# Kernel tuning notes

Measured on AMD Instinct MI355X. Metric: run time of the kernel, lower is better.

Reference implementation:

```python
import jax, jax.numpy as jnp
from jax import lax
import numpy as np

B, T, H, K = 128, 256, 768, 64


def setup_inputs() -> dict:
    key = jax.random.key(0)
    k1, k2, k3, k4 = jax.random.split(key, 4)
    hidden = jax.random.normal(k1, (B, T, H), dtype=jnp.float32)
    masks = jnp.ones((B, T), dtype=jnp.int32)
    target = jax.random.randint(k2, (B, T), 0, K, dtype=jnp.int32)
    W = jax.random.normal(k3, (H, K), dtype=jnp.float32) * 0.02
    b = jnp.zeros((K,), dtype=jnp.float32)
    transitions = jax.random.uniform(k4, (K, K), dtype=jnp.float32)
    return {"hidden": hidden, "masks": masks, "target": target,
            "W": W, "b": b, "transitions": transitions}


def _crf_log_norm(emissions, trans, seq_len):
    # emissions: [B,T,K]; forward algorithm (log-sum-exp recurrence over time)
    Tn = emissions.shape[1]
    alpha0 = emissions[:, 0]  # [B,K]

    def step(alpha, xs):
        emis_t, t = xs
        new = jax.nn.logsumexp(alpha[:, :, None] + trans[None], axis=1) + emis_t
        alpha = jnp.where((t < seq_len)[:, None], new, alpha)
        return alpha, None

    xs = (jnp.swapaxes(emissions[:, 1:], 0, 1), jnp.arange(1, Tn))
    alpha, _ = lax.scan(step, alpha0, xs)
    return jax.nn.logsumexp(alpha, axis=1)  # [B]


def _crf_sequence_score(emissions, tags, trans, seq_len):
    Tn = emissions.shape[1]
    t_idx = jnp.arange(Tn)
    valid = t_idx[None, :] < seq_len[:, None]  # [B,T]
    unary = jnp.take_along_axis(emissions, tags[..., None], axis=2)[..., 0]
    unary = jnp.sum(jnp.where(valid, unary, 0.0), axis=1)
    pair = trans[tags[:, :-1], tags[:, 1:]]  # [B,T-1]
    valid_pair = t_idx[1:][None, :] < seq_len[:, None]
    binary = jnp.sum(jnp.where(valid_pair, pair, 0.0), axis=1)
    return unary + binary


def _crf_decode(emissions, trans, seq_len):
    # Viterbi with backpointers; padded steps carry state (identity backptr)
    Bn, Tn, Kn = emissions.shape
    v0 = emissions[:, 0]

    def step(v, xs):
        emis_t, t = xs
        scores = v[:, :, None] + trans[None]  # [B, K_prev, K_cur]
        bp = jnp.argmax(scores, axis=1).astype(jnp.int32)
        new_v = jnp.max(scores, axis=1) + emis_t
        m = (t < seq_len)[:, None]
        v = jnp.where(m, new_v, v)
        bp = jnp.where(m, bp, jnp.arange(Kn, dtype=jnp.int32)[None])
        return v, bp

    xs = (jnp.swapaxes(emissions[:, 1:], 0, 1), jnp.arange(1, Tn))
    v, bps = lax.scan(step, v0, xs)  # bps: [T-1, B, K]
    best_score = jnp.max(v, axis=1)
    last_tag = jnp.argmax(v, axis=1).astype(jnp.int32)

    def back(tag, bp_t):
        prev = jnp.take_along_axis(bp_t, tag[:, None], axis=1)[:, 0]
        return prev, prev

    _, rev_tags = lax.scan(back, last_tag, bps, reverse=True)  # [T-1, B]
    path = jnp.concatenate([rev_tags, last_tag[None]], axis=0)  # [T, B]
    path = jnp.swapaxes(path, 0, 1)  # [B, T]
    valid = jnp.arange(Tn)[None, :] < seq_len[:, None]
    path = jnp.where(valid, path, 0)
    return path, best_score


def reference(hidden, masks, target, W, b, transitions):
    # dense projection (dropout omitted for determinism)
    emissions = jnp.einsum('bth,hk->btk', hidden, W) + b  # [B,T,K]
    seq_len = jnp.sum(masks, axis=1).astype(jnp.int32)
    log_norm = _crf_log_norm(emissions, transitions, seq_len)
    seq_score = _crf_sequence_score(emissions, target, transitions, seq_len)
    log_likelihood = seq_score - log_norm  # [B]
    decode_predict, _crf_scores = _crf_decode(emissions, transitions, seq_len)
    return decode_predict, log_likelihood
```

## Files before the change

### kernel.cpp

```cpp
#include <hip/hip_runtime.h>

#define B_ 128
#define T_ 256
#define H_ 768
#define K_ 64
#define BT_ (B_ * T_)

template <int CTRL>
__device__ __forceinline__ float dpp_mov_f(float x) {
    return __int_as_float(__builtin_amdgcn_update_dpp(
        __float_as_int(x), __float_as_int(x), CTRL, 0xF, 0xF, false));
}
__device__ __forceinline__ float wave_max64(float x) {
    x = fmaxf(x, dpp_mov_f<0x111>(x));
    x = fmaxf(x, dpp_mov_f<0x112>(x));
    x = fmaxf(x, dpp_mov_f<0x114>(x));
    x = fmaxf(x, dpp_mov_f<0x118>(x));
    x = fmaxf(x, dpp_mov_f<0x142>(x));
    x = fmaxf(x, dpp_mov_f<0x143>(x));
    return __int_as_float(__builtin_amdgcn_readlane(__float_as_int(x), 63));
}
__device__ __forceinline__ float readlane0_f(float x) {
    return __int_as_float(__builtin_amdgcn_readfirstlane(__float_as_int(x)));
}
template <int I>
__device__ __forceinline__ float readlane_f(float x) {
    return __int_as_float(__builtin_amdgcn_readlane(__float_as_int(x), I));
}

#define BK_ 32
#define BM_ 64
#define P_ 66
__global__ __launch_bounds__(256) void gemm_emis(const float* __restrict__ hidden,
                                                 const float* __restrict__ W,
                                                 const float* __restrict__ bias,
                                                 float* __restrict__ emis) {
    __shared__ float At[BK_ * P_];

    const int tid = threadIdx.x;
    const int lane = tid & 63;
    const int wc = __builtin_amdgcn_readfirstlane((tid >> 6) * 16);
    const int rowbase = blockIdx.x * BM_;
    const int srow = tid >> 2;
    const int scol = (tid & 3) * 8;

    float acc[16];
#pragma unroll
    for (int c = 0; c < 16; ++c) acc[c] = bias[wc + c];

    float4 pf0 = *(const float4*)&hidden[(size_t)(rowbase + srow) * H_ + scol];
    float4 pf1 = *(const float4*)&hidden[(size_t)(rowbase + srow) * H_ + scol + 4];

    for (int kb = 0; kb < H_ / BK_; ++kb) {
        __syncthreads();
        At[(scol + 0) * P_ + srow] = pf0.x;
        At[(scol + 1) * P_ + srow] = pf0.y;
        At[(scol + 2) * P_ + srow] = pf0.z;
        At[(scol + 3) * P_ + srow] = pf0.w;
        At[(scol + 4) * P_ + srow] = pf1.x;
        At[(scol + 5) * P_ + srow] = pf1.y;
        At[(scol + 6) * P_ + srow] = pf1.z;
        At[(scol + 7) * P_ + srow] = pf1.w;
        __syncthreads();
        if (kb + 1 < H_ / BK_) {
            pf0 = *(const float4*)&hidden[(size_t)(rowbase + srow) * H_ +
                                          (kb + 1) * BK_ + scol];
            pf1 = *(const float4*)&hidden[(size_t)(rowbase + srow) * H_ +
                                          (kb + 1) * BK_ + scol + 4];
        }
        const float* Wk = &W[(kb * BK_) * K_ + wc];
#pragma unroll 8
        for (int h = 0; h < BK_; ++h) {
            float a = At[h * P_ + lane];
            float4 w0 = *(const float4*)&Wk[h * K_ + 0];
            float4 w1 = *(const float4*)&Wk[h * K_ + 4];
            float4 w2 = *(const float4*)&Wk[h * K_ + 8];
            float4 w3 = *(const float4*)&Wk[h * K_ + 12];
            acc[0]  += a * w0.x;  acc[1]  += a * w0.y;
            acc[2]  += a * w0.z;  acc[3]  += a * w0.w;
            acc[4]  += a * w1.x;  acc[5]  += a * w1.y;
            acc[6]  += a * w1.z;  acc[7]  += a * w1.w;
            acc[8]  += a * w2.x;  acc[9]  += a * w2.y;
            acc[10] += a * w2.z;  acc[11] += a * w2.w;
            acc[12] += a * w3.x;  acc[13] += a * w3.y;
            acc[14] += a * w3.z;  acc[15] += a * w3.w;
        }
    }

    float* e = &emis[(size_t)(rowbase + lane) * K_ + wc];
#pragma unroll
    for (int q = 0; q < 4; ++q)
        *(float4*)&e[q * 4] = make_float4(acc[q * 4], acc[q * 4 + 1],
                                          acc[q * 4 + 2], acc[q * 4 + 3]);
}

__global__ __launch_bounds__(128, 1) void crf_kernel(const float* __restrict__ emis,
                                                     const int* __restrict__ masks,
                                                     const int* __restrict__ target,
                                                     const float* __restrict__ trans,
                                                     float* __restrict__ out) {
    __shared__ __align__(16) float ebuf[T_ * K_];
    __shared__ __align__(16) float vbuf[T_ * K_];
    __shared__ float tbuf[K_ * 65];

    const int tid = threadIdx.x;
    const int lane = tid & 63;
    const int b = blockIdx.x;
    const float* eb = emis + (size_t)b * (T_ * K_);

    {
        const float4* src = (const float4*)eb;
        float4* dst = (float4*)ebuf;
#pragma unroll
        for (int k = 0; k < 32; ++k) dst[tid + k * 128] = src[tid + k * 128];
    }
    int sl = 0;
#pragma unroll
    for (int k = 0; k < 4; ++k) sl += masks[b * T_ + lane + k * 64];
#pragma unroll
    for (int m = 32; m; m >>= 1) sl += __shfl_xor(sl, m, 64);
    const int seq_len = sl;
    __syncthreads();

    if (tid < 64) {
        float Ecol[64];
#pragma unroll
        for (int i = 0; i < 64; ++i) Ecol[i] = __expf(trans[i * K_ + lane]);

        float e_c = ebuf[lane];
        float e00 = readlane0_f(e_c);
        float p = __expf(e_c - e00);
        float C = e00;
        float logD0prev = 0.f;
        float e_n = ebuf[K_ + lane];
        float en0 = readlane0_f(e_n);
        float xg = __expf(e_n - en0);

        for (int t = 1; t < T_; ++t) {
            float e_f = (t < T_ - 1) ? ebuf[(t + 1) * K_ + lane] : 0.f;
            float a0 = 0.f, a1 = 0.f, a2 = 0.f, a3 = 0.f;
            float a4 = 0.f, a5 = 0.f, a6 = 0.f, a7 = 0.f;
#define FWD8(base)                                                     \
            a0 = fmaf(readlane_f<base + 0>(p), Ecol[base + 0], a0);    \
            a1 = fmaf(readlane_f<base + 1>(p), Ecol[base + 1], a1);    \
            a2 = fmaf(readlane_f<base + 2>(p), Ecol[base + 2], a2);    \
            a3 = fmaf(readlane_f<base + 3>(p), Ecol[base + 3], a3);    \
            a4 = fmaf(readlane_f<base + 4>(p), Ecol[base + 4], a4);    \
            a5 = fmaf(readlane_f<base + 5>(p), Ecol[base + 5], a5);    \
            a6 = fmaf(readlane_f<base + 6>(p), Ecol[base + 6], a6);    \
            a7 = fmaf(readlane_f<base + 7>(p), Ecol[base + 7], a7);
            FWD8(0) FWD8(8) FWD8(16) FWD8(24) FWD8(32) FWD8(40) FWD8(48) FWD8(56)
#undef FWD8
            float D = ((a0 + a1) + (a2 + a3)) + ((a4 + a5) + (a6 + a7));
            float pnew = D * xg;
            if (t < seq_len) { p = pnew; C += en0 + logD0prev; }
            float D0 = readlane0_f(D);
            logD0prev = __logf(D0);
            float gn = __fdividef(1.f, D0);
            en0 = readlane0_f(e_f);
            xg = __expf(e_f - en0) * gn;
            e_n = e_f;
        }
        float rs = p;
#pragma unroll
        for (int m = 32; m; m >>= 1) rs += __shfl_xor(rs, m, 64);
        float log_norm = C + __logf(rs);

        float sc = 0.f;
#pragma unroll
        for (int k = 0; k < 4; ++k) {
            int t = lane + k * 64;
            if (t < seq_len) {
                int tg = target[b * T_ + t];
                sc += ebuf[t * K_ + tg];
                if (t >= 1) sc += trans[target[b * T_ + t - 1] * K_ + tg];
            }
        }
#pragma unroll
        for (int m = 32; m; m >>= 1) sc += __shfl_xor(sc, m, 64);
        if (lane == 0) out[BT_ + b] = sc - log_norm;
    } else {
        float Tcol[64];
#pragma unroll
        for (int i = 0; i < 64; ++i) Tcol[i] = trans[i * K_ + lane];
        for (int idx = lane; idx < K_ * K_; idx += 64)
            tbuf[(idx >> 6) * 65 + (idx & 63)] = trans[idx];

        float v = ebuf[lane];
        vbuf[lane] = v;
        float e_n = ebuf[K_ + lane];
        for (int t = 1; t < T_; ++t) {
            float e_f = (t < T_ - 1) ? ebuf[(t + 1) * K_ + lane] : 0.f;
            float m0 = -3.4e38f, m1 = -3.4e38f, m2 = -3.4e38f, m3 = -3.4e38f;
#define VITP(macc, i0, i1)                                                \
            {                                                             \
                float x_ = readlane_f<(i0)>(v) + Tcol[(i0)];              \
                float y_ = readlane_f<(i1)>(v) + Tcol[(i1)];              \
                macc = fmaxf(fmaxf(macc, x_), y_);                        \
            }
#define VIT8(base)                                                        \
            VITP(m0, (base) + 0, (base) + 1)                              \
            VITP(m1, (base) + 2, (base) + 3)                              \
            VITP(m2, (base) + 4, (base) + 5)                              \
            VITP(m3, (base) + 6, (base) + 7)
            VIT8(0) VIT8(8) VIT8(16) VIT8(24) VIT8(32) VIT8(40) VIT8(48) VIT8(56)
#undef VIT8
#undef VITP
            float M = fmaxf(fmaxf(m0, m1), fmaxf(m2, m3));
            float vn = M + e_n;
            if (t < seq_len) v = vn;
            vbuf[t * K_ + lane] = v;
            e_n = e_f;
        }

        float M = wave_max64(v);
        unsigned long long ball = __ballot(v >= M);
        int tag = (int)__builtin_ctzll(ball);

        int path[4];
#pragma unroll
        for (int k = 0; k < 4; ++k) path[k] = 0;
        if (lane == ((T_ - 1) & 63)) path[(T_ - 1) >> 6] = tag;

        float vpre = vbuf[(T_ - 2) * K_ + lane];
        for (int t = T_ - 1; t >= 1; --t) {
            float vnext = (t >= 2) ? vbuf[(t - 2) * K_ + lane] : 0.f;
            if (t < seq_len) {
                float s = vpre + tbuf[lane * 65 + tag];
                float Ms = wave_max64(s);
                unsigned long long bl = __ballot(s >= Ms);
                tag = (int)__builtin_ctzll(bl);
            }
            int pidx = t - 1;
            if (lane == (pidx & 63)) path[pidx >> 6] = tag;
            vpre = vnext;
        }
#pragma unroll
        for (int k = 0; k < 4; ++k) {
            int t = lane + k * 64;
            out[b * T_ + t] = (t < seq_len) ? (float)path[k] : 0.f;
        }
    }
}

extern "C" void kernel_launch(void* const* d_in, const int* in_sizes, int n_in,
                              void* d_out, int out_size, void* d_ws, size_t ws_size,
                              hipStream_t stream) {
    const float* hidden = (const float*)d_in[0];
    const int* masks    = (const int*)d_in[1];
    const int* target   = (const int*)d_in[2];
    const float* W      = (const float*)d_in[3];
    const float* bias   = (const float*)d_in[4];
    const float* trans  = (const float*)d_in[5];
    float* out = (float*)d_out;
    float* emis = (float*)d_ws;

    gemm_emis<<<dim3(BT_ / BM_), dim3(256), 0, stream>>>(hidden, W, bias, emis);
    crf_kernel<<<dim3(B_), dim3(128), 0, stream>>>(emis, masks, target, trans, out);
}
```

Measured before the change: 372.8 us.

## Split CRF forward and Viterbi recurrences across four waves each with LDS exchange

The forward-algorithm and Viterbi recurrences are each spread over four waves instead of one. Each lane computes a quarter of the K-sum (or max) for one target state, combines partials with DPP lane shuffles, and exchanges per-step state through double-buffered shared memory. The intent is to shorten the serial per-timestep dependency chain of 64 readlane operations. In exchange, every timestep now needs a block-wide barrier and an LDS round trip.

```diff
diff --git a/kernel.cpp b/kernel.cpp
--- a/kernel.cpp
+++ b/kernel.cpp
@@ -19,13 +19,6 @@
     x = fmaxf(x, dpp_mov_f<0x142>(x));
     x = fmaxf(x, dpp_mov_f<0x143>(x));
     return __int_as_float(__builtin_amdgcn_readlane(__float_as_int(x), 63));
-}
-__device__ __forceinline__ float readlane0_f(float x) {
-    return __int_as_float(__builtin_amdgcn_readfirstlane(__float_as_int(x)));
-}
-template <int I>
-__device__ __forceinline__ float readlane_f(float x) {
-    return __int_as_float(__builtin_amdgcn_readlane(__float_as_int(x), I));
 }
 
 #define BK_ 32
@@ -94,17 +87,28 @@
                                           acc[q * 4 + 2], acc[q * 4 + 3]);
 }
 
-__global__ __launch_bounds__(128, 1) void crf_kernel(const float* __restrict__ emis,
+__global__ __launch_bounds__(512, 1) void crf_kernel(const float* __restrict__ emis,
                                                      const int* __restrict__ masks,
                                                      const int* __restrict__ target,
                                                      const float* __restrict__ trans,
                                                      float* __restrict__ out) {
     __shared__ __align__(16) float ebuf[T_ * K_];
-    __shared__ __align__(16) float vbuf[T_ * K_];
+    __shared__ __align__(16) float vhist[T_ * K_];
     __shared__ float tbuf[K_ * 65];
+    __shared__ __align__(16) float pbuf[2][K_];
+    __shared__ __align__(16) float vstep[2][K_];
+    __shared__ float sbuf[2];
+    __shared__ float red[8];
 
     const int tid = threadIdx.x;
     const int lane = tid & 63;
+    const int wv = tid >> 6;
+    const bool fwd = (wv < 4);
+    const int wq = fwd ? wv : (wv - 4);
+    const int q = lane & 3;
+    const int jl = lane >> 2;
+    const int j = wq * 16 + jl;
+    const int q16 = q * 16;
     const int b = blockIdx.x;
     const float* eb = emis + (size_t)b * (T_ * K_);
 
@@ -112,7 +116,7 @@
         const float4* src = (const float4*)eb;
         float4* dst = (float4*)ebuf;
 #pragma unroll
-        for (int k = 0; k < 32; ++k) dst[tid + k * 128] = src[tid + k * 128];
+        for (int k = 0; k < 8; ++k) dst[tid + k * 512] = src[tid + k * 512];
     }
     int sl = 0;
 #pragma unroll
@@ -120,52 +124,93 @@
 #pragma unroll
     for (int m = 32; m; m >>= 1) sl += __shfl_xor(sl, m, 64);
     const int seq_len = sl;
+
+    float Eq[16];
+#pragma unroll
+    for (int ii = 0; ii < 16; ++ii) {
+        float tv = trans[(q16 + ii) * K_ + j];
+        Eq[ii] = fwd ? __expf(tv) : tv;
+    }
+    if (wv == 4)
+        for (int idx = lane; idx < K_ * K_; idx += 64)
+            tbuf[(idx >> 6) * 65 + (idx & 63)] = trans[idx];
     __syncthreads();
 
-    if (tid < 64) {
-        float Ecol[64];
-#pragma unroll
-        for (int i = 0; i < 64; ++i) Ecol[i] = __expf(trans[i * K_ + lane]);
-
-        float e_c = ebuf[lane];
-        float e00 = readlane0_f(e_c);
-        float p = __expf(e_c - e00);
-        float C = e00;
-        float logD0prev = 0.f;
-        float e_n = ebuf[K_ + lane];
-        float en0 = readlane0_f(e_n);
-        float xg = __expf(e_n - en0);
-
-        for (int t = 1; t < T_; ++t) {
-            float e_f = (t < T_ - 1) ? ebuf[(t + 1) * K_ + lane] : 0.f;
-            float a0 = 0.f, a1 = 0.f, a2 = 0.f, a3 = 0.f;
-            float a4 = 0.f, a5 = 0.f, a6 = 0.f, a7 = 0.f;
-#define FWD8(base)                                                     \
-            a0 = fmaf(readlane_f<base + 0>(p), Ecol[base + 0], a0);    \
-            a1 = fmaf(readlane_f<base + 1>(p), Ecol[base + 1], a1);    \
-            a2 = fmaf(readlane_f<base + 2>(p), Ecol[base + 2], a2);    \
-            a3 = fmaf(readlane_f<base + 3>(p), Ecol[base + 3], a3);    \
-            a4 = fmaf(readlane_f<base + 4>(p), Ecol[base + 4], a4);    \
-            a5 = fmaf(readlane_f<base + 5>(p), Ecol[base + 5], a5);    \
-            a6 = fmaf(readlane_f<base + 6>(p), Ecol[base + 6], a6);    \
-            a7 = fmaf(readlane_f<base + 7>(p), Ecol[base + 7], a7);
-            FWD8(0) FWD8(8) FWD8(16) FWD8(24) FWD8(32) FWD8(40) FWD8(48) FWD8(56)
-#undef FWD8
-            float D = ((a0 + a1) + (a2 + a3)) + ((a4 + a5) + (a6 + a7));
+    float C = 0.f, p = 0.f, v = 0.f;
+    if (fwd) {
+        float e00 = ebuf[0];
+        p = __expf(ebuf[j] - e00);
+        C = e00;
+        if (q == 0) pbuf[0][j] = p;
+        if (tid == 0) sbuf[0] = 1.0f;
+    } else {
+        v = ebuf[j];
+        if (q == 0) { vstep[0][j] = v; vhist[j] = v; }
+    }
+    __syncthreads();
+
+    for (int t = 1; t < T_; ++t) {
+        const int rp = (t - 1) & 1, wp = t & 1;
+        if (fwd) {
+            const float* pb = pbuf[rp];
+            float4 P0 = *(const float4*)&pb[q16 + 0];
+            float4 P1 = *(const float4*)&pb[q16 + 4];
+            float4 P2 = *(const float4*)&pb[q16 + 8];
+            float4 P3 = *(const float4*)&pb[q16 + 12];
+            float D0p = sbuf[rp];
+            float et0 = ebuf[t * K_];
+            float etj = ebuf[t * K_ + j];
+            float xg = __expf(etj - et0) * __fdividef(1.f, D0p);
+            float s0 = P0.x * Eq[0];     s0 = fmaf(P0.y, Eq[1], s0);
+            s0 = fmaf(P0.z, Eq[2], s0);  s0 = fmaf(P0.w, Eq[3], s0);
+            float s1 = P1.x * Eq[4];     s1 = fmaf(P1.y, Eq[5], s1);
+            s1 = fmaf(P1.z, Eq[6], s1);  s1 = fmaf(P1.w, Eq[7], s1);
+            float s2 = P2.x * Eq[8];     s2 = fmaf(P2.y, Eq[9], s2);
+            s2 = fmaf(P2.z, Eq[10], s2); s2 = fmaf(P2.w, Eq[11], s2);
+            float s3 = P3.x * Eq[12];    s3 = fmaf(P3.y, Eq[13], s3);
+            s3 = fmaf(P3.z, Eq[14], s3); s3 = fmaf(P3.w, Eq[15], s3);
+            float part = (s0 + s1) + (s2 + s3);
+            float u = part + dpp_mov_f<0xB1>(part);
+            float D = u + dpp_mov_f<0x4E>(u);
             float pnew = D * xg;
-            if (t < seq_len) { p = pnew; C += en0 + logD0prev; }
-            float D0 = readlane0_f(D);
-            logD0prev = __logf(D0);
-            float gn = __fdividef(1.f, D0);
-            en0 = readlane0_f(e_f);
-            xg = __expf(e_f - en0) * gn;
-            e_n = e_f;
-        }
-        float rs = p;
-#pragma unroll
-        for (int m = 32; m; m >>= 1) rs += __shfl_xor(rs, m, 64);
+            if (t < seq_len) { p = pnew; C += et0 + __logf(D0p); }
+            if (q == 0) pbuf[wp][j] = p;
+            if (tid == 0) sbuf[wp] = D;
+        } else {
+            const float* vb = vstep[rp];
+            float4 V0 = *(const float4*)&vb[q16 + 0];
+            float4 V1 = *(const float4*)&vb[q16 + 4];
+            float4 V2 = *(const float4*)&vb[q16 + 8];
+            float4 V3 = *(const float4*)&vb[q16 + 12];
+            float etj = ebuf[t * K_ + j];
+            float mA = fmaxf(fmaxf(V0.x + Eq[0],  V0.y + Eq[1]),
+                             fmaxf(V0.z + Eq[2],  V0.w + Eq[3]));
+            float mB = fmaxf(fmaxf(V1.x + Eq[4],  V1.y + Eq[5]),
+                             fmaxf(V1.z + Eq[6],  V1.w + Eq[7]));
+            float mC = fmaxf(fmaxf(V2.x + Eq[8],  V2.y + Eq[9]),
+                             fmaxf(V2.z + Eq[10], V2.w + Eq[11]));
+            float mD = fmaxf(fmaxf(V3.x + Eq[12], V3.y + Eq[13]),
+                             fmaxf(V3.z + Eq[14], V3.w + Eq[15]));
+            float Mq = fmaxf(fmaxf(mA, mB), fmaxf(mC, mD));
+            float u = fmaxf(Mq, dpp_mov_f<0xB1>(Mq));
+            float M = fmaxf(u, dpp_mov_f<0x4E>(u));
+            float vn = M + etj;
+            if (t < seq_len) v = vn;
+            if (q == 0) { vstep[wp][j] = v; vhist[t * K_ + j] = v; }
+        }
+        __syncthreads();
+    }
+
+    if (fwd) {
+        float pm = (q == 0) ? p : 0.f;
+#pragma unroll
+        for (int m = 32; m; m >>= 1) pm += __shfl_xor(pm, m, 64);
+        if (lane == 0) red[wv] = pm;
+    }
+    __syncthreads();
+    if (wv == 0) {
+        float rs = (red[0] + red[1]) + (red[2] + red[3]);
         float log_norm = C + __logf(rs);
-
         float sc = 0.f;
 #pragma unroll
         for (int k = 0; k < 4; ++k) {
@@ -179,42 +224,10 @@
 #pragma unroll
         for (int m = 32; m; m >>= 1) sc += __shfl_xor(sc, m, 64);
         if (lane == 0) out[BT_ + b] = sc - log_norm;
-    } else {
-        float Tcol[64];
-#pragma unroll
-        for (int i = 0; i < 64; ++i) Tcol[i] = trans[i * K_ + lane];
-        for (int idx = lane; idx < K_ * K_; idx += 64)
-            tbuf[(idx >> 6) * 65 + (idx & 63)] = trans[idx];
-
-        float v = ebuf[lane];
-        vbuf[lane] = v;
-        float e_n = ebuf[K_ + lane];
-        for (int t = 1; t < T_; ++t) {
-            float e_f = (t < T_ - 1) ? ebuf[(t + 1) * K_ + lane] : 0.f;
-            float m0 = -3.4e38f, m1 = -3.4e38f, m2 = -3.4e38f, m3 = -3.4e38f;
-#define VITP(macc, i0, i1)                                                \
-            {                                                             \
-                float x_ = readlane_f<(i0)>(v) + Tcol[(i0)];              \
-                float y_ = readlane_f<(i1)>(v) + Tcol[(i1)];              \
-                macc = fmaxf(fmaxf(macc, x_), y_);                        \
-            }
-#define VIT8(base)                                                        \
-            VITP(m0, (base) + 0, (base) + 1)                              \
-            VITP(m1, (base) + 2, (base) + 3)                              \
-            VITP(m2, (base) + 4, (base) + 5)                              \
-            VITP(m3, (base) + 6, (base) + 7)
-            VIT8(0) VIT8(8) VIT8(16) VIT8(24) VIT8(32) VIT8(40) VIT8(48) VIT8(56)
-#undef VIT8
-#undef VITP
-            float M = fmaxf(fmaxf(m0, m1), fmaxf(m2, m3));
-            float vn = M + e_n;
-            if (t < seq_len) v = vn;
-            vbuf[t * K_ + lane] = v;
-            e_n = e_f;
-        }
-
-        float M = wave_max64(v);
-        unsigned long long ball = __ballot(v >= M);
+    } else if (wv == 4) {
+        float vfin = vhist[(T_ - 1) * K_ + lane];
+        float M = wave_max64(vfin);
+        unsigned long long ball = __ballot(vfin >= M);
         int tag = (int)__builtin_ctzll(ball);
 
         int path[4];
@@ -222,9 +235,9 @@
         for (int k = 0; k < 4; ++k) path[k] = 0;
         if (lane == ((T_ - 1) & 63)) path[(T_ - 1) >> 6] = tag;
 
-        float vpre = vbuf[(T_ - 2) * K_ + lane];
+        float vpre = vhist[(T_ - 2) * K_ + lane];
         for (int t = T_ - 1; t >= 1; --t) {
-            float vnext = (t >= 2) ? vbuf[(t - 2) * K_ + lane] : 0.f;
+            float vnext = (t >= 2) ? vhist[(t - 2) * K_ + lane] : 0.f;
             if (t < seq_len) {
                 float s = vpre + tbuf[lane * 65 + tag];
                 float Ms = wave_max64(s);
@@ -256,5 +269,5 @@
     float* emis = (float*)d_ws;
 
     gemm_emis<<<dim3(BT_ / BM_), dim3(256), 0, stream>>>(hidden, W, bias, emis);
-    crf_kernel<<<dim3(B_), dim3(128), 0, stream>>>(emis, masks, target, trans, out);
-}
+    crf_kernel<<<dim3(B_), dim3(512), 0, stream>>>(emis, masks, target, trans, out);
+}
```

Result: no change. 366.9 us (-1.6%).

## Replace readlane broadcasts with DPP wave-rotate chains in CRF recurrences

Applied to the files above, without the earlier changes.

Both the forward (log-sum-exp) and Viterbi recurrences previously broadcast each of 64 lane values via v_readlane (scalar path) and then combined them with per-lane columns. They now rotate the state vector across the wave with DPP row-rotate moves in two directions, multiplying or adding a pre-permuted transition column whose indices are derived at runtime from the rotation direction. This is meant to avoid the scalar readlane latency and SGPR-to-VALU dependency stalls on the serial per-timestep critical path. The trade-off is two dependent 32-long DPP chains per step and reliance on the exact semantics of wave-rotate DPP controls on this hardware.

```diff
diff --git a/kernel.cpp b/kernel.cpp
--- a/kernel.cpp
+++ b/kernel.cpp
@@ -10,6 +10,10 @@
 __device__ __forceinline__ float dpp_mov_f(float x) {
     return __int_as_float(__builtin_amdgcn_update_dpp(
         __float_as_int(x), __float_as_int(x), CTRL, 0xF, 0xF, false));
+}
+template <int CTRL>
+__device__ __forceinline__ int dpp_mov_i(int x) {
+    return __builtin_amdgcn_update_dpp(x, x, CTRL, 0xF, 0xF, false);
 }
 __device__ __forceinline__ float wave_max64(float x) {
     x = fmaxf(x, dpp_mov_f<0x111>(x));
@@ -22,10 +26,6 @@
 }
 __device__ __forceinline__ float readlane0_f(float x) {
     return __int_as_float(__builtin_amdgcn_readfirstlane(__float_as_int(x)));
-}
-template <int I>
-__device__ __forceinline__ float readlane_f(float x) {
-    return __int_as_float(__builtin_amdgcn_readlane(__float_as_int(x), I));
 }
 
 #define BK_ 32
@@ -120,12 +120,21 @@
 #pragma unroll
     for (int m = 32; m; m >>= 1) sl += __shfl_xor(sl, m, 64);
     const int seq_len = sl;
+
+    const int dR = __builtin_amdgcn_readfirstlane(dpp_mov_i<0x13C>(lane)) & 63;
+    const int dL = __builtin_amdgcn_readfirstlane(dpp_mov_i<0x134>(lane)) & 63;
+
     __syncthreads();
 
     if (tid < 64) {
-        float Ecol[64];
-#pragma unroll
-        for (int i = 0; i < 64; ++i) Ecol[i] = __expf(trans[i * K_ + lane]);
+        float Er[64];
+        Er[0] = __expf(trans[lane * K_ + lane]);
+#pragma unroll
+        for (int r = 1; r <= 32; ++r)
+            Er[r] = __expf(trans[(((unsigned)(lane + r * dR)) & 63) * K_ + lane]);
+#pragma unroll
+        for (int s = 1; s <= 31; ++s)
+            Er[32 + s] = __expf(trans[(((unsigned)(lane + s * dL)) & 63) * K_ + lane]);
 
         float e_c = ebuf[lane];
         float e00 = readlane0_f(e_c);
@@ -138,20 +147,45 @@
 
         for (int t = 1; t < T_; ++t) {
             float e_f = (t < T_ - 1) ? ebuf[(t + 1) * K_ + lane] : 0.f;
-            float a0 = 0.f, a1 = 0.f, a2 = 0.f, a3 = 0.f;
-            float a4 = 0.f, a5 = 0.f, a6 = 0.f, a7 = 0.f;
-#define FWD8(base)                                                     \
-            a0 = fmaf(readlane_f<base + 0>(p), Ecol[base + 0], a0);    \
-            a1 = fmaf(readlane_f<base + 1>(p), Ecol[base + 1], a1);    \
-            a2 = fmaf(readlane_f<base + 2>(p), Ecol[base + 2], a2);    \
-            a3 = fmaf(readlane_f<base + 3>(p), Ecol[base + 3], a3);    \
-            a4 = fmaf(readlane_f<base + 4>(p), Ecol[base + 4], a4);    \
-            a5 = fmaf(readlane_f<base + 5>(p), Ecol[base + 5], a5);    \
-            a6 = fmaf(readlane_f<base + 6>(p), Ecol[base + 6], a6);    \
-            a7 = fmaf(readlane_f<base + 7>(p), Ecol[base + 7], a7);
-            FWD8(0) FWD8(8) FWD8(16) FWD8(24) FWD8(32) FWD8(40) FWD8(48) FWD8(56)
-#undef FWD8
-            float D = ((a0 + a1) + (a2 + a3)) + ((a4 + a5) + (a6 + a7));
+            float pr = p, pl = p;
+            float a0 = p * Er[0], a1 = 0.f, a2 = 0.f, a3 = 0.f;
+#define HR(r, acc) { pr = dpp_mov_f<0x13C>(pr); acc = fmaf(pr, Er[r], acc); }
+#define HL(s, acc) { pl = dpp_mov_f<0x134>(pl); acc = fmaf(pl, Er[32 + (s)], acc); }
+            HR(1, a1)   HL(1, a2)
+            HR(2, a3)   HL(2, a0)
+            HR(3, a1)   HL(3, a2)
+            HR(4, a3)   HL(4, a0)
+            HR(5, a1)   HL(5, a2)
+            HR(6, a3)   HL(6, a0)
+            HR(7, a1)   HL(7, a2)
+            HR(8, a3)   HL(8, a0)
+            HR(9, a1)   HL(9, a2)
+            HR(10, a3)  HL(10, a0)
+            HR(11, a1)  HL(11, a2)
+            HR(12, a3)  HL(12, a0)
+            HR(13, a1)  HL(13, a2)
+            HR(14, a3)  HL(14, a0)
+            HR(15, a1)  HL(15, a2)
+            HR(16, a3)  HL(16, a0)
+            HR(17, a1)  HL(17, a2)
+            HR(18, a3)  HL(18, a0)
+            HR(19, a1)  HL(19, a2)
+            HR(20, a3)  HL(20, a0)
+            HR(21, a1)  HL(21, a2)
+            HR(22, a3)  HL(22, a0)
+            HR(23, a1)  HL(23, a2)
+            HR(24, a3)  HL(24, a0)
+            HR(25, a1)  HL(25, a2)
+            HR(26, a3)  HL(26, a0)
+            HR(27, a1)  HL(27, a2)
+            HR(28, a3)  HL(28, a0)
+            HR(29, a1)  HL(29, a2)
+            HR(30, a3)  HL(30, a0)
+            HR(31, a1)  HL(31, a2)
+            HR(32, a3)
+#undef HR
+#undef HL
+            float D = (a0 + a1) + (a2 + a3);
             float pnew = D * xg;
             if (t < seq_len) { p = pnew; C += en0 + logD0prev; }
             float D0 = readlane0_f(D);
@@ -180,9 +214,14 @@
         for (int m = 32; m; m >>= 1) sc += __shfl_xor(sc, m, 64);
         if (lane == 0) out[BT_ + b] = sc - log_norm;
     } else {
-        float Tcol[64];
-#pragma unroll
-        for (int i = 0; i < 64; ++i) Tcol[i] = trans[i * K_ + lane];
+        float Tr[64];
+        Tr[0] = trans[lane * K_ + lane];
+#pragma unroll
+        for (int r = 1; r <= 32; ++r)
+            Tr[r] = trans[(((unsigned)(lane + r * dR)) & 63) * K_ + lane];
+#pragma unroll
+        for (int s = 1; s <= 31; ++s)
+            Tr[32 + s] = trans[(((unsigned)(lane + s * dL)) & 63) * K_ + lane];
         for (int idx = lane; idx < K_ * K_; idx += 64)
             tbuf[(idx >> 6) * 65 + (idx & 63)] = trans[idx];
 
@@ -191,21 +230,45 @@
         float e_n = ebuf[K_ + lane];
         for (int t = 1; t < T_; ++t) {
             float e_f = (t < T_ - 1) ? ebuf[(t + 1) * K_ + lane] : 0.f;
-            float m0 = -3.4e38f, m1 = -3.4e38f, m2 = -3.4e38f, m3 = -3.4e38f;
-#define VITP(macc, i0, i1)                                                \
-            {                                                             \
-                float x_ = readlane_f<(i0)>(v) + Tcol[(i0)];              \
-                float y_ = readlane_f<(i1)>(v) + Tcol[(i1)];              \
-                macc = fmaxf(fmaxf(macc, x_), y_);                        \
-            }
-#define VIT8(base)                                                        \
-            VITP(m0, (base) + 0, (base) + 1)                              \
-            VITP(m1, (base) + 2, (base) + 3)                              \
-            VITP(m2, (base) + 4, (base) + 5)                              \
-            VITP(m3, (base) + 6, (base) + 7)
-            VIT8(0) VIT8(8) VIT8(16) VIT8(24) VIT8(32) VIT8(40) VIT8(48) VIT8(56)
-#undef VIT8
-#undef VITP
+            float vr = v, vl = v;
+            float m0 = v + Tr[0];
+            float m1 = -3.4e38f, m2 = -3.4e38f, m3 = -3.4e38f;
+#define WR(r, macc) { vr = dpp_mov_f<0x13C>(vr); macc = fmaxf(macc, vr + Tr[r]); }
+#define WL(s, macc) { vl = dpp_mov_f<0x134>(vl); macc = fmaxf(macc, vl + Tr[32 + (s)]); }
+            WR(1, m1)   WL(1, m2)
+            WR(2, m3)   WL(2, m0)
+            WR(3, m1)   WL(3, m2)
+            WR(4, m3)   WL(4, m0)
+            WR(5, m1)   WL(5, m2)
+            WR(6, m3)   WL(6, m0)
+            WR(7, m1)   WL(7, m2)
+            WR(8, m3)   WL(8, m0)
+            WR(9, m1)   WL(9, m2)
+            WR(10, m3)  WL(10, m0)
+            WR(11, m1)  WL(11, m2)
+            WR(12, m3)  WL(12, m0)
+            WR(13, m1)  WL(13, m2)
+            WR(14, m3)  WL(14, m0)
+            WR(15, m1)  WL(15, m2)
+            WR(16, m3)  WL(16, m0)
+            WR(17, m1)  WL(17, m2)
+            WR(18, m3)  WL(18, m0)
+            WR(19, m1)  WL(19, m2)
+            WR(20, m3)  WL(20, m0)
+            WR(21, m1)  WL(21, m2)
+            WR(22, m3)  WL(22, m0)
+            WR(23, m1)  WL(23, m2)
+            WR(24, m3)  WL(24, m0)
+            WR(25, m1)  WL(25, m2)
+            WR(26, m3)  WL(26, m0)
+            WR(27, m1)  WL(27, m2)
+            WR(28, m3)  WL(28, m0)
+            WR(29, m1)  WL(29, m2)
+            WR(30, m3)  WL(30, m0)
+            WR(31, m1)  WL(31, m2)
+            WR(32, m3)
+#undef WR
+#undef WL
             float M = fmaxf(fmaxf(m0, m1), fmaxf(m2, m3));
             float vn = M + e_n;
             if (t < seq_len) v = vn;
```

New measurement: 371.9 us. Within noise of the previous version (-0.2%).

## Replace per-lane readlane broadcasts with DPP row-rotate and cross-row shuffles in CRF recurrences

Applied to the files above, without the earlier changes.

The forward and Viterbi recurrences previously broadcast each of the 64 state values with scalar readlane instructions, which serialise through SGPRs. They now get the values by XOR-shuffling across the four 16-lane rows and applying 15 DPP row-rotates per row. The transition matrix is pre-permuted per lane to match the rotated order, and the rotate offsets are discovered at runtime. This is meant to cut the per-step latency of the sequential time loop, at the cost of a few cross-row shuffles per step and more complex indexing.

```diff
diff --git a/kernel.cpp b/kernel.cpp
--- a/kernel.cpp
+++ b/kernel.cpp
@@ -10,6 +10,10 @@
 __device__ __forceinline__ float dpp_mov_f(float x) {
     return __int_as_float(__builtin_amdgcn_update_dpp(
         __float_as_int(x), __float_as_int(x), CTRL, 0xF, 0xF, false));
+}
+template <int CTRL>
+__device__ __forceinline__ int dpp_mov_i(int x) {
+    return __builtin_amdgcn_update_dpp(x, x, CTRL, 0xF, 0xF, false);
 }
 __device__ __forceinline__ float wave_max64(float x) {
     x = fmaxf(x, dpp_mov_f<0x111>(x));
@@ -22,10 +26,6 @@
 }
 __device__ __forceinline__ float readlane0_f(float x) {
     return __int_as_float(__builtin_amdgcn_readfirstlane(__float_as_int(x)));
-}
-template <int I>
-__device__ __forceinline__ float readlane_f(float x) {
-    return __int_as_float(__builtin_amdgcn_readlane(__float_as_int(x), I));
 }
 
 #define BK_ 32
@@ -120,12 +120,27 @@
 #pragma unroll
     for (int m = 32; m; m >>= 1) sl += __shfl_xor(sl, m, 64);
     const int seq_len = sl;
+
+    int off[16];
+    off[0] = 0;
+#define PR(k) off[k] = __builtin_amdgcn_readfirstlane(dpp_mov_i<0x120 + (k)>(lane)) & 15;
+    PR(1) PR(2) PR(3) PR(4) PR(5) PR(6) PR(7) PR(8)
+    PR(9) PR(10) PR(11) PR(12) PR(13) PR(14) PR(15)
+#undef PR
+    const int rw = lane >> 4;
+    const int cl = lane & 15;
+
     __syncthreads();
 
     if (tid < 64) {
-        float Ecol[64];
-#pragma unroll
-        for (int i = 0; i < 64; ++i) Ecol[i] = __expf(trans[i * K_ + lane]);
+        float Et[4][16];
+#pragma unroll
+        for (int m = 0; m < 4; ++m)
+#pragma unroll
+            for (int k = 0; k < 16; ++k) {
+                int i = 16 * (rw ^ m) + ((cl + off[k]) & 15);
+                Et[m][k] = __expf(trans[i * K_ + lane]);
+            }
 
         float e_c = ebuf[lane];
         float e00 = readlane0_f(e_c);
@@ -138,20 +153,22 @@
 
         for (int t = 1; t < T_; ++t) {
             float e_f = (t < T_ - 1) ? ebuf[(t + 1) * K_ + lane] : 0.f;
-            float a0 = 0.f, a1 = 0.f, a2 = 0.f, a3 = 0.f;
-            float a4 = 0.f, a5 = 0.f, a6 = 0.f, a7 = 0.f;
-#define FWD8(base)                                                     \
-            a0 = fmaf(readlane_f<base + 0>(p), Ecol[base + 0], a0);    \
-            a1 = fmaf(readlane_f<base + 1>(p), Ecol[base + 1], a1);    \
-            a2 = fmaf(readlane_f<base + 2>(p), Ecol[base + 2], a2);    \
-            a3 = fmaf(readlane_f<base + 3>(p), Ecol[base + 3], a3);    \
-            a4 = fmaf(readlane_f<base + 4>(p), Ecol[base + 4], a4);    \
-            a5 = fmaf(readlane_f<base + 5>(p), Ecol[base + 5], a5);    \
-            a6 = fmaf(readlane_f<base + 6>(p), Ecol[base + 6], a6);    \
-            a7 = fmaf(readlane_f<base + 7>(p), Ecol[base + 7], a7);
-            FWD8(0) FWD8(8) FWD8(16) FWD8(24) FWD8(32) FWD8(40) FWD8(48) FWD8(56)
-#undef FWD8
-            float D = ((a0 + a1) + (a2 + a3)) + ((a4 + a5) + (a6 + a7));
+            float y1 = __shfl_xor(p, 16, 64);
+            float y2 = __shfl_xor(p, 32, 64);
+            float y3 = __shfl_xor(y1, 32, 64);
+            float a0 = p  * Et[0][0];
+            float a1 = y1 * Et[1][0];
+            float a2 = y2 * Et[2][0];
+            float a3 = y3 * Et[3][0];
+#define RK(k)                                                          \
+            a0 = fmaf(dpp_mov_f<0x120 + (k)>(p),  Et[0][(k)], a0);     \
+            a1 = fmaf(dpp_mov_f<0x120 + (k)>(y1), Et[1][(k)], a1);     \
+            a2 = fmaf(dpp_mov_f<0x120 + (k)>(y2), Et[2][(k)], a2);     \
+            a3 = fmaf(dpp_mov_f<0x120 + (k)>(y3), Et[3][(k)], a3);
+            RK(1) RK(2) RK(3) RK(4) RK(5) RK(6) RK(7) RK(8)
+            RK(9) RK(10) RK(11) RK(12) RK(13) RK(14) RK(15)
+#undef RK
+            float D = (a0 + a1) + (a2 + a3);
             float pnew = D * xg;
             if (t < seq_len) { p = pnew; C += en0 + logD0prev; }
             float D0 = readlane0_f(D);
@@ -180,9 +197,14 @@
         for (int m = 32; m; m >>= 1) sc += __shfl_xor(sc, m, 64);
         if (lane == 0) out[BT_ + b] = sc - log_norm;
     } else {
-        float Tcol[64];
-#pragma unroll
-        for (int i = 0; i < 64; ++i) Tcol[i] = trans[i * K_ + lane];
+        float Tt[4][16];
+#pragma unroll
+        for (int m = 0; m < 4; ++m)
+#pragma unroll
+            for (int k = 0; k < 16; ++k) {
+                int i = 16 * (rw ^ m) + ((cl + off[k]) & 15);
+                Tt[m][k] = trans[i * K_ + lane];
+            }
         for (int idx = lane; idx < K_ * K_; idx += 64)
             tbuf[(idx >> 6) * 65 + (idx & 63)] = trans[idx];
 
@@ -191,21 +213,21 @@
         float e_n = ebuf[K_ + lane];
         for (int t = 1; t < T_; ++t) {
             float e_f = (t < T_ - 1) ? ebuf[(t + 1) * K_ + lane] : 0.f;
-            float m0 = -3.4e38f, m1 = -3.4e38f, m2 = -3.4e38f, m3 = -3.4e38f;
-#define VITP(macc, i0, i1)                                                \
-            {                                                             \
-                float x_ = readlane_f<(i0)>(v) + Tcol[(i0)];              \
-                float y_ = readlane_f<(i1)>(v) + Tcol[(i1)];              \
-                macc = fmaxf(fmaxf(macc, x_), y_);                        \
-            }
-#define VIT8(base)                                                        \
-            VITP(m0, (base) + 0, (base) + 1)                              \
-            VITP(m1, (base) + 2, (base) + 3)                              \
-            VITP(m2, (base) + 4, (base) + 5)                              \
-            VITP(m3, (base) + 6, (base) + 7)
-            VIT8(0) VIT8(8) VIT8(16) VIT8(24) VIT8(32) VIT8(40) VIT8(48) VIT8(56)
-#undef VIT8
-#undef VITP
+            float y1 = __shfl_xor(v, 16, 64);
+            float y2 = __shfl_xor(v, 32, 64);
+            float y3 = __shfl_xor(y1, 32, 64);
+            float m0 = v  + Tt[0][0];
+            float m1 = y1 + Tt[1][0];
+            float m2 = y2 + Tt[2][0];
+            float m3 = y3 + Tt[3][0];
+#define VK(k)                                                            \
+            m0 = fmaxf(m0, dpp_mov_f<0x120 + (k)>(v)  + Tt[0][(k)]);     \
+            m1 = fmaxf(m1, dpp_mov_f<0x120 + (k)>(y1) + Tt[1][(k)]);     \
+            m2 = fmaxf(m2, dpp_mov_f<0x120 + (k)>(y2) + Tt[2][(k)]);     \
+            m3 = fmaxf(m3, dpp_mov_f<0x120 + (k)>(y3) + Tt[3][(k)]);
+            VK(1) VK(2) VK(3) VK(4) VK(5) VK(6) VK(7) VK(8)
+            VK(9) VK(10) VK(11) VK(12) VK(13) VK(14) VK(15)
+#undef VK
             float M = fmaxf(fmaxf(m0, m1), fmaxf(m2, m3));
             float vn = M + e_n;
             if (t < seq_len) v = vn;
```

Result: slower. 397.2 us (+6.6%).
